# Kernel optimization log

Measured on AMD Instinct MI355X. Metric: run time of the kernel, lower is better.

## Reference

```python
import jax, jax.numpy as jnp
import numpy as np

R, C = 9, 9  # local window (rows, cols)


def setup_inputs() -> dict:
    key = jax.random.key(0)
    k1, k2, k3, k4, k5 = jax.random.split(key, 5)
    q = jax.random.normal(k1, (8, 256, 128, 128), jnp.float32)      # (B, q_size, H, W)
    c_t = jax.random.normal(k2, (8, 256, 512), jnp.float32)          # (B, T, c_size)
    W_a = jax.random.normal(k3, (512, 256), jnp.float32) * 0.04      # Linear(q_size -> c_size), no bias
    W_p = jax.random.normal(k4, (256, 512), jnp.float32) * 0.04      # Linear(c_size -> p_size)
    V_p = jax.random.normal(k5, (2, 256), jnp.float32) * 0.06        # Linear(p_size -> 2)
    return {"q": q, "c_t": c_t, "W_a": W_a, "W_p": W_p, "V_p": V_p}


def reference(q, c_t, W_a, W_p, V_p):
    B, D, H, W = q.shape
    T = c_t.shape[1]
    S = H  # q.size(2) before padding

    # predictive alignment: p_t = S * sigmoid(V_p(tanh(W_p(c_t))))  -> (B, T, 2)
    p_t = S * jax.nn.sigmoid(jnp.tanh(c_t @ W_p.T) @ V_p.T)

    # pad top/left with NaN, flatten spatial dims
    qp = jnp.pad(q, ((0, 0), (0, 0), (1, 0), (1, 0)), constant_values=jnp.nan)
    rows, cols = H + 1, W + 1
    qf = qp.reshape(B, D, rows * cols).transpose(0, 2, 1)  # (B, rows*cols, D)

    roff = jnp.arange(-(R // 2), (R + 1) // 2)  # R offsets
    coff = jnp.arange(-(C // 2), (C + 1) // 2)  # C offsets
    r = jnp.clip(jnp.round(p_t[..., 0]).astype(jnp.int32)[..., None] + roff + 1, 0, rows) % rows  # (B,T,R)
    c = jnp.clip(jnp.round(p_t[..., 1]).astype(jnp.int32)[..., None] + coff + 1, 0, cols) % cols  # (B,T,C)

    # flat window indices, order i*C + j (matches torch stack order)
    s = (r[..., :, None] * cols + c[..., None, :]).reshape(B, T, R * C)

    # gather windows: (B, T, R*C, D)
    qg = jnp.take_along_axis(qf, s.reshape(B, T * R * C, 1), axis=1).reshape(B, T, R * C, D)
    nan_loc = jnp.isnan(qg[..., 0])                    # (B, T, R*C)
    qg = jnp.where(nan_loc[..., None], 0.0, qg)

    # Gaussian positional weighting
    rexp = -2.0 * ((jnp.clip(r - 1, 0, None).astype(jnp.float32) - p_t[..., 0:1]) / (R // 2)) ** 2
    cexp = -2.0 * ((jnp.clip(c - 1, 0, None).astype(jnp.float32) - p_t[..., 1:2]) / (C // 2)) ** 2
    gauss = jnp.exp((rexp[..., :, None] + cexp[..., None, :]).reshape(B, T, R * C))

    # score: (W_a q) . c_t  -> (B, T, R*C)
    a_t = jnp.einsum('btkd,cd,btc->btk', qg, W_a, c_t)
    a_t = jnp.where(nan_loc, -jnp.inf, a_t)
    W_attn = jax.nn.softmax(a_t, axis=2) * gauss

    out = jnp.einsum('btk,btkd->btd', W_attn, qg)  # (B, T, D)
    return out
```

## Files before the change

### kernel.cpp

```cpp
#include <hip/hip_runtime.h>
#include <math.h>

#define Bq 8
#define Tt 256
#define Dd 256
#define Hh 128
#define Ww 128
#define Cc 512
#define HW (Hh*Ww)
#define NBT (Bq*Tt)

__global__ __launch_bounds__(256) void transpose_wp(
    const float* __restrict__ W_p, float* __restrict__ WpT)
{
    __shared__ float tile[32][33];
    const int bx = blockIdx.x;
    const int by = blockIdx.y;
    const int lx = threadIdx.x & 31, ly = threadIdx.x >> 5;
#pragma unroll
    for (int j = 0; j < 4; j++) {
        int p = by * 32 + ly + j * 8;
        tile[ly + j * 8][lx] = W_p[(size_t)p * Cc + bx * 32 + lx];
    }
    __syncthreads();
#pragma unroll
    for (int j = 0; j < 4; j++) {
        int c = bx * 32 + ly + j * 8;
        WpT[(size_t)c * 256 + by * 32 + lx] = tile[lx][ly + j * 8];
    }
}

#define TOK 8
__global__ __launch_bounds__(512) void prep_kernel(
    const float* __restrict__ c_t,
    const float* __restrict__ W_a,
    const float* __restrict__ WpT,
    const float* __restrict__ V_p,
    float* __restrict__ u_ws,
    float* __restrict__ p_ws)
{
    __shared__ float y0s[TOK][256];
    __shared__ float y1s[TOK][256];
    const int tid  = threadIdx.x;
    const int o    = tid & 255;
    const int half = tid >> 8;
    const int bt0  = blockIdx.x * TOK;

    const float* Wcol = (half ? WpT : W_a) + o;
    const float* ct0  = c_t + (size_t)bt0 * Cc;

    float acc[TOK];
#pragma unroll
    for (int t = 0; t < TOK; t++) acc[t] = 0.f;

    for (int c = 0; c < Cc; c += 8) {
        float w0 = Wcol[(size_t)(c + 0) * 256];
        float w1 = Wcol[(size_t)(c + 1) * 256];
        float w2 = Wcol[(size_t)(c + 2) * 256];
        float w3 = Wcol[(size_t)(c + 3) * 256];
        float w4 = Wcol[(size_t)(c + 4) * 256];
        float w5 = Wcol[(size_t)(c + 5) * 256];
        float w6 = Wcol[(size_t)(c + 6) * 256];
        float w7 = Wcol[(size_t)(c + 7) * 256];
#pragma unroll
        for (int t = 0; t < TOK; t++) {
            const float* r = ct0 + t * Cc + c;
            acc[t] = fmaf(r[0], w0, acc[t]);
            acc[t] = fmaf(r[1], w1, acc[t]);
            acc[t] = fmaf(r[2], w2, acc[t]);
            acc[t] = fmaf(r[3], w3, acc[t]);
            acc[t] = fmaf(r[4], w4, acc[t]);
            acc[t] = fmaf(r[5], w5, acc[t]);
            acc[t] = fmaf(r[6], w6, acc[t]);
            acc[t] = fmaf(r[7], w7, acc[t]);
        }
    }

    if (half == 0) {
#pragma unroll
        for (int t = 0; t < TOK; t++)
            u_ws[(size_t)(bt0 + t) * Dd + o] = acc[t];
    } else {
        float v0 = V_p[o], v1 = V_p[256 + o];
#pragma unroll
        for (int t = 0; t < TOK; t++) {
            float th = tanhf(acc[t]);
            y0s[t][o] = th * v0;
            y1s[t][o] = th * v1;
        }
    }
    __syncthreads();

    const int wv = tid >> 6, ln = tid & 63;
    float s0 = y0s[wv][ln] + y0s[wv][ln + 64] + y0s[wv][ln + 128] + y0s[wv][ln + 192];
    float s1 = y1s[wv][ln] + y1s[wv][ln + 64] + y1s[wv][ln + 128] + y1s[wv][ln + 192];
#pragma unroll
    for (int of = 32; of >= 1; of >>= 1) {
        s0 += __shfl_xor(s0, of);
        s1 += __shfl_xor(s1, of);
    }
    if (ln == 0) {
        p_ws[(size_t)(bt0 + wv) * 2 + 0] = 128.f / (1.f + expf(-s0));
        p_ws[(size_t)(bt0 + wv) * 2 + 1] = 128.f / (1.f + expf(-s1));
    }
}

__global__ __launch_bounds__(256) void attn_kernel(
    const float* __restrict__ q,
    const float* __restrict__ u_ws,
    const float* __restrict__ p_ws,
    float* __restrict__ out)
{
    __shared__ __align__(16) _Float16 win[Dd][9][12];
    __shared__ float u_s[Dd];
    __shared__ float a_red[243];
    __shared__ float w_s[81];
    __shared__ float a_s[81];
    __shared__ float e_s[81];
    __shared__ float rex_s[9], cex_s[9];
    __shared__ int   rr_s[9], cc_s[9];
    __shared__ float m_sh, inv_sh;

    const int tid = threadIdx.x;
    int bt = blockIdx.x;
    bt = ((bt & 7) << 8) | (bt >> 3);
    const int b = bt >> 8;

    u_s[tid] = u_ws[(size_t)bt * Dd + tid];

    {
        float4* wf = (float4*)&win[0][0][0];
        for (int i = tid; i < (int)(sizeof(win) / 16); i += 256) {
            wf[i] = make_float4(0.f, 0.f, 0.f, 0.f);
        }
    }

    if (tid < 18) {
        int   i = (tid < 9) ? tid : tid - 9;
        float p = p_ws[(size_t)bt * 2 + ((tid < 9) ? 0 : 1)];
        int base = (int)rintf(p);
        int v = base + i - 3;
        v = min(max(v, 0), 129) % 129;
        float cl = (float)max(v - 1, 0);
        float z  = (cl - p) * 0.25f;
        float ex = -2.f * z * z;
        if (tid < 9) { rr_s[i] = v; rex_s[i] = ex; }
        else         { cc_s[i] = v; cex_s[i] = ex; }
    }
    __syncthreads();

    int jc0 = 0, c0 = 1;
#pragma unroll
    for (int j = 8; j >= 0; j--)
        if (cc_s[j] > 0) { jc0 = j; c0 = cc_s[j]; }
    const int cb = min((c0 - 1) & ~3, Ww - 12);
    const int e0 = (c0 - 1) - cb;

    {
        const int g  = tid >> 5;
        const int l5 = tid & 31;
        const bool lact = (l5 < 27);
        const int li = lact ? ((l5 * 171) >> 9) : 0;
        const int lv = l5 - li * 3;
        const int vr = lact ? rr_s[li] : 0;
        const int rowoff = (max(vr, 1) - 1) * Ww + cb + 4 * lv;
        const float* qb = q + (size_t)b * Dd * HW;
        if (lact && vr > 0) {
            for (int dd = 0; dd < Dd; dd += 32) {
                const int d0 = dd + g;
                float4 x0 = *(const float4*)(qb + (size_t)(d0     ) * HW + rowoff);
                float4 x1 = *(const float4*)(qb + (size_t)(d0 +  8) * HW + rowoff);
                float4 x2 = *(const float4*)(qb + (size_t)(d0 + 16) * HW + rowoff);
                float4 x3 = *(const float4*)(qb + (size_t)(d0 + 24) * HW + rowoff);
                union { _Float16 h[4]; uint2 u; } p0, p1, p2, p3;
                p0.h[0] = (_Float16)x0.x; p0.h[1] = (_Float16)x0.y;
                p0.h[2] = (_Float16)x0.z; p0.h[3] = (_Float16)x0.w;
                p1.h[0] = (_Float16)x1.x; p1.h[1] = (_Float16)x1.y;
                p1.h[2] = (_Float16)x1.z; p1.h[3] = (_Float16)x1.w;
                p2.h[0] = (_Float16)x2.x; p2.h[1] = (_Float16)x2.y;
                p2.h[2] = (_Float16)x2.z; p2.h[3] = (_Float16)x2.w;
                p3.h[0] = (_Float16)x3.x; p3.h[1] = (_Float16)x3.y;
                p3.h[2] = (_Float16)x3.z; p3.h[3] = (_Float16)x3.w;
                *(uint2*)&win[d0     ][li][4 * lv] = p0.u;
                *(uint2*)&win[d0 +  8][li][4 * lv] = p1.u;
                *(uint2*)&win[d0 + 16][li][4 * lv] = p2.u;
                *(uint2*)&win[d0 + 24][li][4 * lv] = p3.u;
            }
        }
    }
    __syncthreads();

    if (tid < 243) {
        const int k  = tid % 81;
        const int s  = tid / 81;
        const int ki = (k * 57) >> 9;
        const int kj = k - ki * 9;
        const int pos = min(max(e0 + kj - jc0, 0), 11);
        const _Float16* wp = &win[0][ki][pos];
        float ap = 0.f;
        int d = s;
        if (s == 0) {
            ap = fmaf((float)wp[0], u_s[0], ap);
            d = 3;
        }
        const _Float16* w = wp + (size_t)d * 108;
        for (int it = 0; it < 17; it++) {
            float x0 = (float)w[0];
            float x1 = (float)w[3 * 108];
            float x2 = (float)w[6 * 108];
            float x3 = (float)w[9 * 108];
            float x4 = (float)w[12 * 108];
            ap = fmaf(x0, u_s[d     ], ap);
            ap = fmaf(x1, u_s[d + 3 ], ap);
            ap = fmaf(x2, u_s[d + 6 ], ap);
            ap = fmaf(x3, u_s[d + 9 ], ap);
            ap = fmaf(x4, u_s[d + 12], ap);
            w += 15 * 108;
            d += 15;
        }
        a_red[tid] = ap;
    }
    __syncthreads();

    float a_val = -INFINITY;
    bool  valid_k = false;
    if (tid < 81) {
        const int ki = (tid * 57) >> 9;
        const int kj = tid - ki * 9;
        valid_k = (rr_s[ki] > 0) && (cc_s[kj] > 0);
        float a = a_red[tid] + a_red[tid + 81] + a_red[tid + 162];
        a_val = valid_k ? a : -INFINITY;
        a_s[tid] = a_val;
    }
    __syncthreads();

    if (tid < 64) {
        float m = a_s[tid];
        if (tid + 64 < 81) m = fmaxf(m, a_s[tid + 64]);
        for (int o = 32; o >= 1; o >>= 1) m = fmaxf(m, __shfl_xor(m, o));
        if (tid == 0) m_sh = m;
    }
    __syncthreads();
    {
        float e = 0.f;
        if (tid < 81 && valid_k) e = expf(a_val - m_sh);
        if (tid < 81) e_s[tid] = e;
    }
    __syncthreads();
    if (tid < 64) {
        float sv = e_s[tid] + ((tid + 64 < 81) ? e_s[tid + 64] : 0.f);
        for (int o = 32; o >= 1; o >>= 1) sv += __shfl_xor(sv, o);
        if (tid == 0) inv_sh = 1.f / sv;
    }
    __syncthreads();
    if (tid < 81) {
        int i = (tid * 57) >> 9;
        int j = tid - i * 9;
        float g = expf(rex_s[i] + cex_s[j]);
        w_s[tid] = e_s[tid] * inv_sh * g;
    }
    __syncthreads();

    int posj[9];
#pragma unroll
    for (int j = 0; j < 9; j++) posj[j] = min(max(e0 + j - jc0, 0), 11);
    const _Float16* wd = &win[tid][0][0];
    float acc = 0.f;
#pragma unroll
    for (int k = 0; k < 81; k++) {
        const int ki = k / 9, kj = k % 9;
        acc = fmaf(w_s[k], (float)wd[ki * 12 + posj[kj]], acc);
    }
    out[(size_t)bt * Dd + tid] = acc;
}

extern "C" void kernel_launch(void* const* d_in, const int* in_sizes, int n_in,
                              void* d_out, int out_size, void* d_ws, size_t ws_size,
                              hipStream_t stream) {
    const float* q   = (const float*)d_in[0];
    const float* c_t = (const float*)d_in[1];
    const float* W_a = (const float*)d_in[2];
    const float* W_p = (const float*)d_in[3];
    const float* V_p = (const float*)d_in[4];
    float* out  = (float*)d_out;
    float* u_ws = (float*)d_ws;
    float* p_ws = u_ws + (size_t)NBT * Dd;
    float* WpT  = p_ws + (size_t)NBT * 2;

    transpose_wp<<<dim3(16, 8), 256, 0, stream>>>(W_p, WpT);
    prep_kernel<<<NBT / TOK, 512, 0, stream>>>(c_t, W_a, WpT, V_p, u_ws, p_ws);
    attn_kernel<<<NBT, 256, 0, stream>>>(q, u_ws, p_ws, out);
}
```

Measured before the change: 267.8 us.

## Fuse score dot-product into window gather and broadcast c_t via readlane

In the attention kernel, the q·u score is now accumulated in fp32 while the window is being loaded from global memory. Per-group partials are kept in shared memory and reduced over 108 window positions, which replaces a separate pass that re-read the fp16 window from shared memory. This removes a shared-memory sweep and a sync phase, and scores are now computed from fp32 values rather than fp16-rounded ones. In the prep kernel, TOK drops to 4 and c_t values are held in registers and broadcast with readlane instead of being read repeatedly from global memory; this doubles the block count and adds a prefetch of the next chunk.

```diff
diff --git a/kernel.cpp b/kernel.cpp
--- a/kernel.cpp
+++ b/kernel.cpp
@@ -10,6 +10,10 @@
 #define HW (Hh*Ww)
 #define NBT (Bq*Tt)
 
+__device__ __forceinline__ float lane_bcast(float x, int l) {
+    return __uint_as_float(__builtin_amdgcn_readlane(__float_as_uint(x), l));
+}
+
 __global__ __launch_bounds__(256) void transpose_wp(
     const float* __restrict__ W_p, float* __restrict__ WpT)
 {
@@ -30,7 +34,7 @@
     }
 }
 
-#define TOK 8
+#define TOK 4
 __global__ __launch_bounds__(512) void prep_kernel(
     const float* __restrict__ c_t,
     const float* __restrict__ W_a,
@@ -44,36 +48,41 @@
     const int tid  = threadIdx.x;
     const int o    = tid & 255;
     const int half = tid >> 8;
+    const int ln   = tid & 63;
     const int bt0  = blockIdx.x * TOK;
 
     const float* Wcol = (half ? WpT : W_a) + o;
-    const float* ct0  = c_t + (size_t)bt0 * Cc;
+    const float* ctb  = c_t + (size_t)bt0 * Cc;
 
     float acc[TOK];
 #pragma unroll
     for (int t = 0; t < TOK; t++) acc[t] = 0.f;
 
-    for (int c = 0; c < Cc; c += 8) {
-        float w0 = Wcol[(size_t)(c + 0) * 256];
-        float w1 = Wcol[(size_t)(c + 1) * 256];
-        float w2 = Wcol[(size_t)(c + 2) * 256];
-        float w3 = Wcol[(size_t)(c + 3) * 256];
-        float w4 = Wcol[(size_t)(c + 4) * 256];
-        float w5 = Wcol[(size_t)(c + 5) * 256];
-        float w6 = Wcol[(size_t)(c + 6) * 256];
-        float w7 = Wcol[(size_t)(c + 7) * 256];
-#pragma unroll
-        for (int t = 0; t < TOK; t++) {
-            const float* r = ct0 + t * Cc + c;
-            acc[t] = fmaf(r[0], w0, acc[t]);
-            acc[t] = fmaf(r[1], w1, acc[t]);
-            acc[t] = fmaf(r[2], w2, acc[t]);
-            acc[t] = fmaf(r[3], w3, acc[t]);
-            acc[t] = fmaf(r[4], w4, acc[t]);
-            acc[t] = fmaf(r[5], w5, acc[t]);
-            acc[t] = fmaf(r[6], w6, acc[t]);
-            acc[t] = fmaf(r[7], w7, acc[t]);
-        }
+    float ctr[TOK], ctn[TOK];
+#pragma unroll
+    for (int t = 0; t < TOK; t++) ctr[t] = ctb[t * Cc + ln];
+
+#pragma unroll
+    for (int c0 = 0; c0 < Cc; c0 += 64) {
+        if (c0 + 64 < Cc) {
+#pragma unroll
+            for (int t = 0; t < TOK; t++) ctn[t] = ctb[t * Cc + c0 + 64 + ln];
+        }
+#pragma unroll
+        for (int cc8 = 0; cc8 < 64; cc8 += 8) {
+            float w[8];
+#pragma unroll
+            for (int j = 0; j < 8; j++)
+                w[j] = Wcol[(size_t)(c0 + cc8 + j) * 256];
+#pragma unroll
+            for (int j = 0; j < 8; j++) {
+#pragma unroll
+                for (int t = 0; t < TOK; t++)
+                    acc[t] = fmaf(lane_bcast(ctr[t], cc8 + j), w[j], acc[t]);
+            }
+        }
+#pragma unroll
+        for (int t = 0; t < TOK; t++) ctr[t] = ctn[t];
     }
 
     if (half == 0) {
@@ -91,18 +100,14 @@
     }
     __syncthreads();
 
-    const int wv = tid >> 6, ln = tid & 63;
-    float s0 = y0s[wv][ln] + y0s[wv][ln + 64] + y0s[wv][ln + 128] + y0s[wv][ln + 192];
-    float s1 = y1s[wv][ln] + y1s[wv][ln + 64] + y1s[wv][ln + 128] + y1s[wv][ln + 192];
-#pragma unroll
-    for (int of = 32; of >= 1; of >>= 1) {
-        s0 += __shfl_xor(s0, of);
-        s1 += __shfl_xor(s1, of);
-    }
-    if (ln == 0) {
-        p_ws[(size_t)(bt0 + wv) * 2 + 0] = 128.f / (1.f + expf(-s0));
-        p_ws[(size_t)(bt0 + wv) * 2 + 1] = 128.f / (1.f + expf(-s1));
-    }
+    const int wv = tid >> 6;
+    const int t  = wv & 3;
+    const float* ys = (wv < 4) ? &y0s[t][0] : &y1s[t][0];
+    float s = ys[ln] + ys[ln + 64] + ys[ln + 128] + ys[ln + 192];
+#pragma unroll
+    for (int of = 32; of >= 1; of >>= 1) s += __shfl_xor(s, of);
+    if (ln == 0)
+        p_ws[(size_t)(bt0 + t) * 2 + ((wv < 4) ? 0 : 1)] = 128.f / (1.f + expf(-s));
 }
 
 __global__ __launch_bounds__(256) void attn_kernel(
@@ -112,8 +117,9 @@
     float* __restrict__ out)
 {
     __shared__ __align__(16) _Float16 win[Dd][9][12];
+    __shared__ __align__(16) float pacc_s[8][9][12];
+    __shared__ float ascore[9][12];
     __shared__ float u_s[Dd];
-    __shared__ float a_red[243];
     __shared__ float w_s[81];
     __shared__ float a_s[81];
     __shared__ float e_s[81];
@@ -130,9 +136,9 @@
 
     {
         float4* wf = (float4*)&win[0][0][0];
-        for (int i = tid; i < (int)(sizeof(win) / 16); i += 256) {
-            wf[i] = make_float4(0.f, 0.f, 0.f, 0.f);
-        }
+        for (int i = tid; i < 3456; i += 256) wf[i] = make_float4(0.f, 0.f, 0.f, 0.f);
+        float* pz = &pacc_s[0][0][0];
+        for (int i = tid; i < 864; i += 256) pz[i] = 0.f;
     }
 
     if (tid < 18) {
@@ -166,12 +172,22 @@
         const int rowoff = (max(vr, 1) - 1) * Ww + cb + 4 * lv;
         const float* qb = q + (size_t)b * Dd * HW;
         if (lact && vr > 0) {
+            float px = 0.f, py = 0.f, pz = 0.f, pw = 0.f;
             for (int dd = 0; dd < Dd; dd += 32) {
                 const int d0 = dd + g;
                 float4 x0 = *(const float4*)(qb + (size_t)(d0     ) * HW + rowoff);
                 float4 x1 = *(const float4*)(qb + (size_t)(d0 +  8) * HW + rowoff);
                 float4 x2 = *(const float4*)(qb + (size_t)(d0 + 16) * HW + rowoff);
                 float4 x3 = *(const float4*)(qb + (size_t)(d0 + 24) * HW + rowoff);
+                float u0 = u_s[d0], u1 = u_s[d0 + 8], u2 = u_s[d0 + 16], u3 = u_s[d0 + 24];
+                px = fmaf(x0.x, u0, px); py = fmaf(x0.y, u0, py);
+                pz = fmaf(x0.z, u0, pz); pw = fmaf(x0.w, u0, pw);
+                px = fmaf(x1.x, u1, px); py = fmaf(x1.y, u1, py);
+                pz = fmaf(x1.z, u1, pz); pw = fmaf(x1.w, u1, pw);
+                px = fmaf(x2.x, u2, px); py = fmaf(x2.y, u2, py);
+                pz = fmaf(x2.z, u2, pz); pw = fmaf(x2.w, u2, pw);
+                px = fmaf(x3.x, u3, px); py = fmaf(x3.y, u3, py);
+                pz = fmaf(x3.z, u3, pz); pw = fmaf(x3.w, u3, pw);
                 union { _Float16 h[4]; uint2 u; } p0, p1, p2, p3;
                 p0.h[0] = (_Float16)x0.x; p0.h[1] = (_Float16)x0.y;
                 p0.h[2] = (_Float16)x0.z; p0.h[3] = (_Float16)x0.w;
@@ -186,39 +202,18 @@
                 *(uint2*)&win[d0 + 16][li][4 * lv] = p2.u;
                 *(uint2*)&win[d0 + 24][li][4 * lv] = p3.u;
             }
-        }
-    }
-    __syncthreads();
-
-    if (tid < 243) {
-        const int k  = tid % 81;
-        const int s  = tid / 81;
-        const int ki = (k * 57) >> 9;
-        const int kj = k - ki * 9;
-        const int pos = min(max(e0 + kj - jc0, 0), 11);
-        const _Float16* wp = &win[0][ki][pos];
-        float ap = 0.f;
-        int d = s;
-        if (s == 0) {
-            ap = fmaf((float)wp[0], u_s[0], ap);
-            d = 3;
-        }
-        const _Float16* w = wp + (size_t)d * 108;
-        for (int it = 0; it < 17; it++) {
-            float x0 = (float)w[0];
-            float x1 = (float)w[3 * 108];
-            float x2 = (float)w[6 * 108];
-            float x3 = (float)w[9 * 108];
-            float x4 = (float)w[12 * 108];
-            ap = fmaf(x0, u_s[d     ], ap);
-            ap = fmaf(x1, u_s[d + 3 ], ap);
-            ap = fmaf(x2, u_s[d + 6 ], ap);
-            ap = fmaf(x3, u_s[d + 9 ], ap);
-            ap = fmaf(x4, u_s[d + 12], ap);
-            w += 15 * 108;
-            d += 15;
-        }
-        a_red[tid] = ap;
+            *(float4*)&pacc_s[g][li][4 * lv] = make_float4(px, py, pz, pw);
+        }
+    }
+    __syncthreads();
+
+    if (tid < 108) {
+        const int li  = tid / 12;
+        const int pos = tid - li * 12;
+        float s = 0.f;
+#pragma unroll
+        for (int g = 0; g < 8; g++) s += pacc_s[g][li][pos];
+        ascore[li][pos] = s;
     }
     __syncthreads();
 
@@ -228,8 +223,8 @@
         const int ki = (tid * 57) >> 9;
         const int kj = tid - ki * 9;
         valid_k = (rr_s[ki] > 0) && (cc_s[kj] > 0);
-        float a = a_red[tid] + a_red[tid + 81] + a_red[tid + 162];
-        a_val = valid_k ? a : -INFINITY;
+        const int pos = min(max(e0 + kj - jc0, 0), 11);
+        a_val = valid_k ? ascore[ki][pos] : -INFINITY;
         a_s[tid] = a_val;
     }
     __syncthreads();
```

After: 264.0 us. Within noise of the previous version (-1.4%).
